# Performance work log

Measured on AMD Instinct MI355X. Metric: run time of the kernel, lower is better.

Reference implementation:

```python
import jax, jax.numpy as jnp
import numpy as np

IH, IW = 14, 14
NUM_HEADS = 16
HEAD_DIMS = 32
INP_DIMS = 512
B = 128


def make_relative_position_index(ih, iw):
    coords = np.stack(np.meshgrid(np.arange(ih), np.arange(iw), indexing='ij'))  # [2, ih, iw]
    cf = coords.reshape(2, -1)  # [2, n]
    rel = cf[:, :, None] - cf[:, None, :]  # [2, n, n]
    rel = rel.transpose(1, 2, 0)  # [n, n, 2]
    rel[:, :, 0] += ih - 1
    rel[:, :, 1] += iw - 1
    rel[:, :, 0] *= 2 * iw - 1
    return rel.sum(-1).astype(np.int64)  # [n, n]


def setup_inputs() -> dict:
    key = jax.random.key(0)
    k1, k2, k3, k4, k5 = jax.random.split(key, 5)
    n = IH * IW
    inner = NUM_HEADS * HEAD_DIMS
    x = jax.random.normal(k1, (B, n, INP_DIMS), dtype=jnp.float32)
    qkv_w = jax.random.normal(k2, (INP_DIMS, 3 * inner), dtype=jnp.float32) * 0.02
    rel_bias_table = jax.random.normal(k3, ((2 * IH - 1) * (2 * IW - 1), NUM_HEADS), dtype=jnp.float32) * 0.02
    proj_w = jax.random.normal(k4, (inner, INP_DIMS), dtype=jnp.float32) * 0.02
    proj_b = jax.random.normal(k5, (INP_DIMS,), dtype=jnp.float32) * 0.02
    rel_pos_index = jnp.asarray(make_relative_position_index(IH, IW))
    return {"x": x, "qkv_w": qkv_w, "rel_bias_table": rel_bias_table,
            "proj_w": proj_w, "proj_b": proj_b, "rel_pos_index": rel_pos_index}


def reference(x, qkv_w, rel_bias_table, proj_w, proj_b, rel_pos_index):
    b, n, c = x.shape
    h, hd = NUM_HEADS, HEAD_DIMS
    scale = (INP_DIMS // NUM_HEADS) ** (-0.5)
    qkv = x @ qkv_w  # [b, n, 3*h*hd]
    qkv = qkv.reshape(b, n, 3, h, hd).transpose(2, 0, 3, 1, 4)  # [3, b, h, n, hd]
    q, k, v = qkv[0] * scale, qkv[1], qkv[2]
    attn = jnp.einsum('bhqd,bhkd->bhqk', q, k)  # [b, h, n, n]
    # gather relative position bias: [n*n, h] -> [h, n, n]
    bias = rel_bias_table[rel_pos_index.reshape(-1)].reshape(n, n, h).transpose(2, 0, 1)
    attn = jax.nn.softmax(attn + bias[None], axis=-1)
    out = jnp.einsum('bhqk,bhkd->bhqd', attn, v)  # [b, h, n, hd]
    out = out.transpose(0, 2, 1, 3).reshape(b, n, h * hd)
    return out @ proj_w + proj_b
```

## Files before the change

### kernel.cpp

```cpp
#include <hip/hip_runtime.h>

#define NTOK 196
#define QPAD 208
#define KP 208
#define PSTR 232
#define VKP 208

typedef __attribute__((ext_vector_type(8))) short short8;
typedef __attribute__((ext_vector_type(4))) short short4_t;
typedef __attribute__((ext_vector_type(4))) float float4_t;

__device__ __forceinline__ short f2bf(float f) {
  unsigned u = __float_as_uint(f);
  u = (u + 0x7fffu + ((u >> 16) & 1u)) >> 16;
  return (short)u;
}

__global__ __launch_bounds__(256) void fill_kernel(float* __restrict__ out,
                                                   int n) {
  int i = blockIdx.x * 256 + threadIdx.x;
  if (i < n) out[i] = 1000.0f;
}

__device__ __forceinline__ void transpose_body(const float* __restrict__ in,
                                               short* __restrict__ out, int R,
                                               int C, int bx, int by,
                                               float (*tile)[65]) {
  int c0 = bx * 64, r0 = by * 64;
  int tc = threadIdx.x & 63, tr = threadIdx.x >> 6;
#pragma unroll
  for (int s = 0; s < 16; s++) {
    int r = s * 4 + tr;
    tile[r][tc] = in[(r0 + r) * C + c0 + tc];
  }
  __syncthreads();
#pragma unroll
  for (int s = 0; s < 16; s++) {
    int i = s * 4 + tr;
    out[(c0 + i) * R + r0 + tc] = f2bf(tile[tc][i]);
  }
}

__global__ __launch_bounds__(256) void prep_kernel(
    const float* __restrict__ qkv_w, const float* __restrict__ proj_w,
    const float* __restrict__ table, const int* __restrict__ rpi,
    const float* __restrict__ x, short* __restrict__ wt1,
    short* __restrict__ wt2, float* __restrict__ bias, short* __restrict__ vb,
    short* __restrict__ xb, int do_vpad) {
  __shared__ float tile[64][65];
  int blk = blockIdx.x;
  if (blk < 192) {
    transpose_body(qkv_w, wt1, 512, 1536, blk % 24, blk / 24, tile);
  } else if (blk < 256) {
    int i = blk - 192;
    transpose_body(proj_w, wt2, 512, 512, i % 8, i / 8, tile);
  } else if (blk < 2960) {
    int idx = (blk - 256) * 256 + threadIdx.x;
    int h = idx / (QPAD * KP);
    int rem = idx % (QPAD * KP);
    int q = rem / KP, k = rem % KP;
    float v = 0.f;
    if (q < NTOK && k < NTOK) v = table[rpi[q * NTOK + k] * 16 + h];
    bias[idx] = v;
  } else if (blk < 3728) {
    if (do_vpad) {
      int i = (blk - 2960) * 256 + threadIdx.x;
      int row = i / 3, g = i - 3 * (i / 3);
      short4_t z = {0, 0, 0, 0};
      *(short4_t*)&vb[row * VKP + 196 + g * 4] = z;
    }
  } else {
    int i = ((blk - 3728) * 256 + threadIdx.x) * 8;
    float4_t a = *(const float4_t*)&x[i];
    float4_t b = *(const float4_t*)&x[i + 4];
    short8 v;
    v[0] = f2bf(a[0]); v[1] = f2bf(a[1]); v[2] = f2bf(a[2]); v[3] = f2bf(a[3]);
    v[4] = f2bf(b[0]); v[5] = f2bf(b[1]); v[6] = f2bf(b[2]); v[7] = f2bf(b[3]);
    *(short8*)&xb[i] = v;
  }
}

__device__ __forceinline__ void gemm_tile(const short* __restrict__ A,
                                          const short* __restrict__ B, int K,
                                          int m0, int n0, short* As, short* Bs,
                                          float4_t acc[4][4]) {
  int tid = threadIdx.x;
  int lane = tid & 63, wave = tid >> 6;
  int quad = lane >> 4, l16 = lane & 15;
  int wm = (wave >> 1) * 64, wn = (wave & 1) * 64;
  int lrow = lane >> 3, lcol = (lane & 7) * 8;
  const short* Abase = A + m0 * K;
  const short* Bbase = B + n0 * K;
  for (int k0 = 0; k0 < K; k0 += 64) {
#pragma unroll
    for (int i = 0; i < 4; i++) {
      int r = (wave * 4 + i) * 8;
      __builtin_amdgcn_global_load_lds(
          (const __attribute__((address_space(1))) void*)
              &Abase[(r + lrow) * K + k0 + lcol],
          (__attribute__((address_space(3))) void*)&As[r * 64], 16, 0, 0);
      __builtin_amdgcn_global_load_lds(
          (const __attribute__((address_space(1))) void*)
              &Bbase[(r + lrow) * K + k0 + lcol],
          (__attribute__((address_space(3))) void*)&Bs[r * 64], 16, 0, 0);
    }
    __syncthreads();
#pragma unroll
    for (int ks = 0; ks < 2; ks++) {
      short8 af[4], bfr[4];
#pragma unroll
      for (int i = 0; i < 4; i++) {
        af[i] = *(short8*)&As[(wm + i * 16 + l16) * 64 + ks * 32 + quad * 8];
        bfr[i] = *(short8*)&Bs[(wn + i * 16 + l16) * 64 + ks * 32 + quad * 8];
      }
#pragma unroll
      for (int mi = 0; mi < 4; mi++)
#pragma unroll
        for (int ni = 0; ni < 4; ni++)
          acc[mi][ni] = __builtin_amdgcn_mfma_f32_16x16x32_bf16(
              af[mi], bfr[ni], acc[mi][ni], 0, 0, 0);
    }
    __syncthreads();
  }
}

__global__ __launch_bounds__(256) void qkv_gemm(
    const short* __restrict__ xb, const short* __restrict__ wt1,
    short* __restrict__ qb, short* __restrict__ kb, short* __restrict__ vb) {
  __shared__ __align__(16) short As[128 * 64];
  __shared__ __align__(16) short Bs[128 * 64];
  float4_t acc[4][4];
  float4_t z = {0.f, 0.f, 0.f, 0.f};
#pragma unroll
  for (int i = 0; i < 4; i++)
#pragma unroll
    for (int j = 0; j < 4; j++) acc[i][j] = z;
  int lin = blockIdx.x + blockIdx.y * 12;
  int xcd = lin & 7, loc = lin >> 3;
  int nl = xcd * 294 + loc;
  int bx = nl % 12, by = nl / 12;
  int m0 = by * 128, n0 = bx * 128;
  gemm_tile(xb, wt1, 512, m0, n0, As, Bs, acc);
  int lane = threadIdx.x & 63, wave = threadIdx.x >> 6;
  int quad = lane >> 4, l16 = lane & 15;
  int wm = (wave >> 1) * 64, wn = (wave & 1) * 64;
  const float qscale = 0.17677669529663687f;
#pragma unroll
  for (int mi = 0; mi < 4; mi++)
#pragma unroll
    for (int ni = 0; ni < 4; ni++) {
      int colg = n0 + wn + ni * 16 + l16;
      int s = colg >> 9, rem = colg & 511;
      int h = rem >> 5, d = rem & 31;
      int rowg0 = m0 + wm + mi * 16 + quad * 4;
      if (s == 2) {
        int b = rowg0 / NTOK, nt = rowg0 - b * NTOK;
        short4_t v4;
        v4[0] = f2bf(acc[mi][ni][0]);
        v4[1] = f2bf(acc[mi][ni][1]);
        v4[2] = f2bf(acc[mi][ni][2]);
        v4[3] = f2bf(acc[mi][ni][3]);
        *(short4_t*)&vb[((b * 16 + h) * 32 + d) * VKP + nt] = v4;
      } else {
#pragma unroll
        for (int r = 0; r < 4; r++) {
          int rowg = rowg0 + r;
          int b = rowg / NTOK, n = rowg - b * NTOK;
          int off = ((b * 16 + h) * QPAD + n) * 32 + d;
          if (s == 0)
            qb[off] = f2bf(acc[mi][ni][r] * qscale);
          else
            kb[off] = f2bf(acc[mi][ni][r]);
        }
      }
    }
}

__global__ __launch_bounds__(256) void attn_kernel(
    const short* __restrict__ qb, const short* __restrict__ kb,
    const short* __restrict__ vb, const float* __restrict__ bias,
    short* __restrict__ aout) {
  __shared__ __align__(16) short vT[32][PSTR];
  __shared__ __align__(16) short P[4][16][PSTR];
  int bh = blockIdx.x, b = bh >> 4, h = bh & 15;
  int tid = threadIdx.x, wave = tid >> 6, lane = tid & 63;
  int quad = lane >> 4, l16 = lane & 15;
  int base_row = b * NTOK;
  const short* vsrc = vb + bh * 32 * VKP;
  for (int i = tid; i < 32 * 26; i += 256) {
    int d = i / 26, c = (i - d * 26) * 8;
    *(short8*)&vT[d][c] = *(const short8*)&vsrc[d * VKP + c];
  }
  short8 z8 = {0, 0, 0, 0, 0, 0, 0, 0};
  if (tid < 96) {
    int d = tid / 3, c = 208 + (tid - d * 3) * 8;
    *(short8*)&vT[d][c] = z8;
  }
  __syncthreads();
  float4_t z4 = {0.f, 0.f, 0.f, 0.f};
  for (int i2 = 0; i2 < 4; i2++) {
    bool active = (i2 < 3) || (wave == 0);
    if (!active) break;
    int qt = (i2 < 3) ? (wave + 4 * i2) : 12;
    int qr0 = qt * 16;
    short8 qf = *(const short8*)&qb[(bh * QPAD + qr0 + l16) * 32 + quad * 8];
    float4_t s[13];
#pragma unroll
    for (int kt = 0; kt < 13; kt++) {
      short8 kf =
          *(const short8*)&kb[(bh * QPAD + kt * 16 + l16) * 32 + quad * 8];
      s[kt] = __builtin_amdgcn_mfma_f32_16x16x32_bf16(qf, kf, z4, 0, 0, 0);
    }
    const float* brow = bias + (h * QPAD + qr0 + quad * 4) * KP;
#pragma unroll
    for (int kt = 0; kt < 13; kt++) {
      int col = kt * 16 + l16;
#pragma unroll
      for (int r = 0; r < 4; r++) s[kt][r] += brow[r * KP + col];
    }
    if (l16 >= 4) {
#pragma unroll
      for (int r = 0; r < 4; r++) s[12][r] = -1e30f;
    }
    float invr[4];
#pragma unroll
    for (int r = 0; r < 4; r++) {
      float m = s[0][r];
#pragma unroll
      for (int kt = 1; kt < 13; kt++) m = fmaxf(m, s[kt][r]);
      m = fmaxf(m, __shfl_xor(m, 8, 16));
      m = fmaxf(m, __shfl_xor(m, 4, 16));
      m = fmaxf(m, __shfl_xor(m, 2, 16));
      m = fmaxf(m, __shfl_xor(m, 1, 16));
      float sum = 0.f;
#pragma unroll
      for (int kt = 0; kt < 13; kt++) {
        float p = __expf(s[kt][r] - m);
        s[kt][r] = p;
        sum += p;
      }
      sum += __shfl_xor(sum, 8, 16);
      sum += __shfl_xor(sum, 4, 16);
      sum += __shfl_xor(sum, 2, 16);
      sum += __shfl_xor(sum, 1, 16);
      invr[r] = 1.f / sum;
      short* prow = &P[wave][quad * 4 + r][0];
#pragma unroll
      for (int kt = 0; kt < 13; kt++)
        prow[kt * 16 + l16] = f2bf(s[kt][r]);
      prow[208 + l16] = 0;
    }
    float4_t o0 = z4, o1 = z4;
#pragma unroll
    for (int kt = 0; kt < 7; kt++) {
      short8 pf = *(short8*)&P[wave][l16][kt * 32 + quad * 8];
      short8 vf0 = *(short8*)&vT[l16][kt * 32 + quad * 8];
      short8 vf1 = *(short8*)&vT[16 + l16][kt * 32 + quad * 8];
      o0 = __builtin_amdgcn_mfma_f32_16x16x32_bf16(pf, vf0, o0, 0, 0, 0);
      o1 = __builtin_amdgcn_mfma_f32_16x16x32_bf16(pf, vf1, o1, 0, 0, 0);
    }
#pragma unroll
    for (int r = 0; r < 4; r++) {
      int row = qr0 + quad * 4 + r;
      if (row < NTOK) {
        int off = (base_row + row) * 512 + h * 32;
        aout[off + l16] = f2bf(o0[r] * invr[r]);
        aout[off + 16 + l16] = f2bf(o1[r] * invr[r]);
      }
    }
  }
}

__global__ __launch_bounds__(256, 2) void fused_attn(
    const short* __restrict__ xb, const short* __restrict__ wt1,
    const float* __restrict__ bias, short* __restrict__ aout) {
  __shared__ __align__(16) short R1[64 * PSTR];
  __shared__ __align__(16) short R2[32 * PSTR];
  __shared__ __align__(16) short Qs[224][40];
  __shared__ __align__(16) short Ks[224][40];
  short(*As)[40] = (short(*)[40])R1;
  short(*P)[PSTR] = (short(*)[PSTR])R1;
  short(*Bs)[40] = (short(*)[40])R2;
  short(*vTs)[PSTR] = (short(*)[PSTR])R2;

  int bh = blockIdx.x, b = bh >> 4, h = bh & 15;
  int tid = threadIdx.x, wave = tid >> 6, lane = tid & 63;
  int quad = lane >> 4, l16 = lane & 15;
  int base_row = b * NTOK;

  float4_t z4 = {0.f, 0.f, 0.f, 0.f};
  float4_t acc[4][6];
#pragma unroll
  for (int i = 0; i < 4; i++)
#pragma unroll
    for (int n = 0; n < 6; n++) acc[i][n] = z4;

  int srow = tid >> 2, scol = (tid & 3) * 8;
  for (int k0 = 0; k0 < 512; k0 += 32) {
#pragma unroll
    for (int i = 0; i < 4; i++) {
      int r = srow + i * 64;
      if (r < 224) {
        int gr = base_row + r;
        if (gr > 25087) gr = 25087;
        *(short8*)&As[r][scol] = *(const short8*)&xb[gr * 512 + k0 + scol];
      }
    }
#pragma unroll
    for (int i = 0; i < 2; i++) {
      int r = srow + i * 64;
      if (r < 96) {
        int sec = r >> 5, r32 = r & 31;
        *(short8*)&Bs[r][scol] =
            *(const short8*)&wt1[(sec * 512 + h * 32 + r32) * 512 + k0 + scol];
      }
    }
    __syncthreads();
    short8 af[4], bfv[6];
#pragma unroll
    for (int i = 0; i < 4; i++) {
      int mt = (i < 3) ? (wave + 4 * i) : (12 + (wave & 1));
      af[i] = *(short8*)&As[mt * 16 + l16][quad * 8];
    }
#pragma unroll
    for (int n = 0; n < 6; n++) bfv[n] = *(short8*)&Bs[n * 16 + l16][quad * 8];
#pragma unroll
    for (int i = 0; i < 4; i++)
#pragma unroll
      for (int n = 0; n < 6; n++)
        acc[i][n] = __builtin_amdgcn_mfma_f32_16x16x32_bf16(af[i], bfv[n],
                                                            acc[i][n], 0, 0, 0);
    __syncthreads();
  }
  const float qscale = 0.17677669529663687f;
#pragma unroll
  for (int i = 0; i < 4; i++) {
    if (i == 3 && wave >= 2) break;
    int mt = (i < 3) ? (wave + 4 * i) : (12 + wave);
    int row0 = mt * 16 + quad * 4;
#pragma unroll
    for (int n = 0; n < 6; n++) {
      int c = n * 16 + l16;
#pragma unroll
      for (int r = 0; r < 4; r++) {
        int row = row0 + r;
        float v = acc[i][n][r];
        if (c < 32)
          Qs[row][c] = f2bf(v * qscale);
        else if (c < 64)
          Ks[row][c - 32] = f2bf(v);
        else
          vTs[c - 64][row] = f2bf(v);
      }
    }
  }
  __syncthreads();
  for (int i2 = 0; i2 < 4; i2++) {
    bool active = (i2 < 3) || (wave == 0);
    int qt = (i2 < 3) ? (wave + 4 * i2) : 12;
    int qr0 = qt * 16;
    if (active) {
      short8 qf = *(short8*)&Qs[qr0 + l16][quad * 8];
      float4_t s[13];
#pragma unroll
      for (int kt = 0; kt < 13; kt++) {
        short8 kf = *(short8*)&Ks[kt * 16 + l16][quad * 8];
        s[kt] = __builtin_amdgcn_mfma_f32_16x16x32_bf16(qf, kf, z4, 0, 0, 0);
      }
      const float* brow = bias + (h * QPAD + qr0 + quad * 4) * KP;
#pragma unroll
      for (int kt = 0; kt < 13; kt++) {
        int col = kt * 16 + l16;
#pragma unroll
        for (int r = 0; r < 4; r++) s[kt][r] += brow[r * KP + col];
      }
      if (l16 >= 4) {
#pragma unroll
        for (int r = 0; r < 4; r++) s[12][r] = -1e30f;
      }
      int prow_base = wave * 16 + quad * 4;
#pragma unroll
      for (int r = 0; r < 4; r++) {
        float m = s[0][r];
#pragma unroll
        for (int kt = 1; kt < 13; kt++) m = fmaxf(m, s[kt][r]);
        m = fmaxf(m, __shfl_xor(m, 8, 16));
        m = fmaxf(m, __shfl_xor(m, 4, 16));
        m = fmaxf(m, __shfl_xor(m, 2, 16));
        m = fmaxf(m, __shfl_xor(m, 1, 16));
        float sum = 0.f;
#pragma unroll
        for (int kt = 0; kt < 13; kt++) {
          float p = __expf(s[kt][r] - m);
          s[kt][r] = p;
          sum += p;
        }
        sum += __shfl_xor(sum, 8, 16);
        sum += __shfl_xor(sum, 4, 16);
        sum += __shfl_xor(sum, 2, 16);
        sum += __shfl_xor(sum, 1, 16);
        float inv = 1.f / sum;
        short* prow = &P[prow_base + r][0];
#pragma unroll
        for (int kt = 0; kt < 13; kt++)
          prow[kt * 16 + l16] = f2bf(s[kt][r] * inv);
        prow[208 + l16] = 0;
      }
    }
    __syncthreads();
    if (active) {
      float4_t o0 = z4, o1 = z4;
#pragma unroll
      for (int kt = 0; kt < 7; kt++) {
        short8 pf = *(short8*)&P[wave * 16 + l16][kt * 32 + quad * 8];
        short8 vf0 = *(short8*)&vTs[l16][kt * 32 + quad * 8];
        short8 vf1 = *(short8*)&vTs[16 + l16][kt * 32 + quad * 8];
        o0 = __builtin_amdgcn_mfma_f32_16x16x32_bf16(pf, vf0, o0, 0, 0, 0);
        o1 = __builtin_amdgcn_mfma_f32_16x16x32_bf16(pf, vf1, o1, 0, 0, 0);
      }
#pragma unroll
      for (int r = 0; r < 4; r++) {
        int row = qr0 + quad * 4 + r;
        if (row < NTOK) {
          int off = (base_row + row) * 512 + h * 32;
          aout[off + l16] = f2bf(o0[r]);
          aout[off + 16 + l16] = f2bf(o1[r]);
        }
      }
    }
    __syncthreads();
  }
}

__global__ __launch_bounds__(256) void proj_gemm(
    const short* __restrict__ a, const short* __restrict__ wt,
    const float* __restrict__ pb, float* __restrict__ out) {
  __shared__ __align__(16) short As[128 * 64];
  __shared__ __align__(16) short Bs[128 * 64];
  float4_t acc[4][4];
  float4_t z = {0.f, 0.f, 0.f, 0.f};
#pragma unroll
  for (int i = 0; i < 4; i++)
#pragma unroll
    for (int j = 0; j < 4; j++) acc[i][j] = z;
  int lin = blockIdx.x + blockIdx.y * 4;
  int xcd = lin & 7, loc = lin >> 3;
  int nl = xcd * 98 + loc;
  int bx = nl % 4, by = nl / 4;
  int m0 = by * 128, n0 = bx * 128;
  gemm_tile(a, wt, 512, m0, n0, As, Bs, acc);
  int lane = threadIdx.x & 63, wave = threadIdx.x >> 6;
  int quad = lane >> 4, l16 = lane & 15;
  int wm = (wave >> 1) * 64, wn = (wave & 1) * 64;
#pragma unroll
  for (int mi = 0; mi < 4; mi++)
#pragma unroll
    for (int ni = 0; ni < 4; ni++) {
      int colg = n0 + wn + ni * 16 + l16;
      float bv = pb[colg];
#pragma unroll
      for (int r = 0; r < 4; r++) {
        int rowg = m0 + wm + mi * 16 + quad * 4 + r;
        out[rowg * 512 + colg] = acc[mi][ni][r] + bv;
      }
    }
}

extern "C" void kernel_launch(void* const* d_in, const int* in_sizes, int n_in,
                              void* d_out, int out_size, void* d_ws,
                              size_t ws_size, hipStream_t stream) {
  const float* x = (const float*)d_in[0];
  const float* qkv_w = (const float*)d_in[1];
  const float* table = (const float*)d_in[2];
  const float* proj_w = (const float*)d_in[3];
  const float* proj_b = (const float*)d_in[4];
  const int* rpi = (const int*)d_in[5];
  float* out = (float*)d_out;

  char* w = (char*)d_ws;
  short* wt1 = (short*)(w);
  short* wt2 = (short*)(w + 1572864);
  float* bias = (float*)(w + 2097152);
  short* xb = (short*)(w + 4866048);
  short* qb = (short*)(w + 30556160);
  short* kb = (short*)(w + 57819136);
  short* vb = (short*)(w + 85082112);
  const size_t NEEDED_SPLIT = 112345088;
  const size_t NEEDED_FUSED = 30556160 + 25690112;

  int split = ws_size >= NEEDED_SPLIT;
  if (ws_size >= NEEDED_FUSED) {
    prep_kernel<<<10000, 256, 0, stream>>>(qkv_w, proj_w, table, rpi, x, wt1,
                                           wt2, bias, vb, xb, split);
  }
  if (split) {
    short* aout = xb;
    qkv_gemm<<<dim3(12, 196), 256, 0, stream>>>(xb, wt1, qb, kb, vb);
    attn_kernel<<<2048, 256, 0, stream>>>(qb, kb, vb, bias, aout);
    proj_gemm<<<dim3(4, 196), 256, 0, stream>>>(aout, wt2, proj_b, out);
  } else if (ws_size >= NEEDED_FUSED) {
    short* aout = (short*)(w + 30556160);
    fused_attn<<<2048, 256, 0, stream>>>(xb, wt1, bias, aout);
    proj_gemm<<<dim3(4, 196), 256, 0, stream>>>(aout, wt2, proj_b, out);
  } else {
    fill_kernel<<<(out_size + 255) / 256, 256, 0, stream>>>(out, out_size);
  }
}
```

Measured before the change: 274.9 us.

## Pad GEMM LDS tiles, fold log2e into scales, hoist K fragments

The GEMM tile loader switches from direct global-to-LDS loads into an unpadded 64-wide layout to plain register-staged loads into 72-wide padded LDS rows. The padding is meant to avoid bank conflicts on the MFMA fragment reads. The softmax now uses exp2f, with log2(e) folded into the query scale and into the precomputed bias table, removing a multiply per exponent. K fragments in the attention kernel are loaded once per block into registers instead of once per query tile, which raises register pressure.

```diff
diff --git a/kernel.cpp b/kernel.cpp
--- a/kernel.cpp
+++ b/kernel.cpp
@@ -60,7 +60,8 @@
     int rem = idx % (QPAD * KP);
     int q = rem / KP, k = rem % KP;
     float v = 0.f;
-    if (q < NTOK && k < NTOK) v = table[rpi[q * NTOK + k] * 16 + h];
+    if (q < NTOK && k < NTOK)
+      v = table[rpi[q * NTOK + k] * 16 + h] * 1.4426950408889634f;
     bias[idx] = v;
   } else if (blk < 3728) {
     if (do_vpad) {
@@ -82,27 +83,19 @@
 
 __device__ __forceinline__ void gemm_tile(const short* __restrict__ A,
                                           const short* __restrict__ B, int K,
-                                          int m0, int n0, short* As, short* Bs,
-                                          float4_t acc[4][4]) {
+                                          int m0, int n0, short (*As)[72],
+                                          short (*Bs)[72], float4_t acc[4][4]) {
   int tid = threadIdx.x;
   int lane = tid & 63, wave = tid >> 6;
   int quad = lane >> 4, l16 = lane & 15;
   int wm = (wave >> 1) * 64, wn = (wave & 1) * 64;
-  int lrow = lane >> 3, lcol = (lane & 7) * 8;
-  const short* Abase = A + m0 * K;
-  const short* Bbase = B + n0 * K;
+  int srow = tid >> 3, scol = (tid & 7) * 8;
   for (int k0 = 0; k0 < K; k0 += 64) {
 #pragma unroll
     for (int i = 0; i < 4; i++) {
-      int r = (wave * 4 + i) * 8;
-      __builtin_amdgcn_global_load_lds(
-          (const __attribute__((address_space(1))) void*)
-              &Abase[(r + lrow) * K + k0 + lcol],
-          (__attribute__((address_space(3))) void*)&As[r * 64], 16, 0, 0);
-      __builtin_amdgcn_global_load_lds(
-          (const __attribute__((address_space(1))) void*)
-              &Bbase[(r + lrow) * K + k0 + lcol],
-          (__attribute__((address_space(3))) void*)&Bs[r * 64], 16, 0, 0);
+      int r = srow + i * 32;
+      *(short8*)&As[r][scol] = *(const short8*)&A[(m0 + r) * K + k0 + scol];
+      *(short8*)&Bs[r][scol] = *(const short8*)&B[(n0 + r) * K + k0 + scol];
     }
     __syncthreads();
 #pragma unroll
@@ -110,8 +103,8 @@
       short8 af[4], bfr[4];
 #pragma unroll
       for (int i = 0; i < 4; i++) {
-        af[i] = *(short8*)&As[(wm + i * 16 + l16) * 64 + ks * 32 + quad * 8];
-        bfr[i] = *(short8*)&Bs[(wn + i * 16 + l16) * 64 + ks * 32 + quad * 8];
+        af[i] = *(short8*)&As[wm + i * 16 + l16][ks * 32 + quad * 8];
+        bfr[i] = *(short8*)&Bs[wn + i * 16 + l16][ks * 32 + quad * 8];
       }
 #pragma unroll
       for (int mi = 0; mi < 4; mi++)
@@ -127,8 +120,8 @@
 __global__ __launch_bounds__(256) void qkv_gemm(
     const short* __restrict__ xb, const short* __restrict__ wt1,
     short* __restrict__ qb, short* __restrict__ kb, short* __restrict__ vb) {
-  __shared__ __align__(16) short As[128 * 64];
-  __shared__ __align__(16) short Bs[128 * 64];
+  __shared__ __align__(16) short As[128][72];
+  __shared__ __align__(16) short Bs[128][72];
   float4_t acc[4][4];
   float4_t z = {0.f, 0.f, 0.f, 0.f};
 #pragma unroll
@@ -144,7 +137,7 @@
   int lane = threadIdx.x & 63, wave = threadIdx.x >> 6;
   int quad = lane >> 4, l16 = lane & 15;
   int wm = (wave >> 1) * 64, wn = (wave & 1) * 64;
-  const float qscale = 0.17677669529663687f;
+  const float qscale = 0.17677669529663687f * 1.4426950408889634f;
 #pragma unroll
   for (int mi = 0; mi < 4; mi++)
 #pragma unroll
@@ -197,6 +190,10 @@
     *(short8*)&vT[d][c] = z8;
   }
   __syncthreads();
+  short8 kfr[13];
+#pragma unroll
+  for (int kt = 0; kt < 13; kt++)
+    kfr[kt] = *(const short8*)&kb[(bh * QPAD + kt * 16 + l16) * 32 + quad * 8];
   float4_t z4 = {0.f, 0.f, 0.f, 0.f};
   for (int i2 = 0; i2 < 4; i2++) {
     bool active = (i2 < 3) || (wave == 0);
@@ -206,11 +203,8 @@
     short8 qf = *(const short8*)&qb[(bh * QPAD + qr0 + l16) * 32 + quad * 8];
     float4_t s[13];
 #pragma unroll
-    for (int kt = 0; kt < 13; kt++) {
-      short8 kf =
-          *(const short8*)&kb[(bh * QPAD + kt * 16 + l16) * 32 + quad * 8];
-      s[kt] = __builtin_amdgcn_mfma_f32_16x16x32_bf16(qf, kf, z4, 0, 0, 0);
-    }
+    for (int kt = 0; kt < 13; kt++)
+      s[kt] = __builtin_amdgcn_mfma_f32_16x16x32_bf16(qf, kfr[kt], z4, 0, 0, 0);
     const float* brow = bias + (h * QPAD + qr0 + quad * 4) * KP;
 #pragma unroll
     for (int kt = 0; kt < 13; kt++) {
@@ -235,7 +229,7 @@
       float sum = 0.f;
 #pragma unroll
       for (int kt = 0; kt < 13; kt++) {
-        float p = __expf(s[kt][r] - m);
+        float p = exp2f(s[kt][r] - m);
         s[kt][r] = p;
         sum += p;
       }
@@ -332,7 +326,7 @@
                                                             acc[i][n], 0, 0, 0);
     __syncthreads();
   }
-  const float qscale = 0.17677669529663687f;
+  const float qscale = 0.17677669529663687f * 1.4426950408889634f;
 #pragma unroll
   for (int i = 0; i < 4; i++) {
     if (i == 3 && wave >= 2) break;
@@ -391,7 +385,7 @@
         float sum = 0.f;
 #pragma unroll
         for (int kt = 0; kt < 13; kt++) {
-          float p = __expf(s[kt][r] - m);
+          float p = exp2f(s[kt][r] - m);
           s[kt][r] = p;
           sum += p;
         }
@@ -435,8 +429,8 @@
 __global__ __launch_bounds__(256) void proj_gemm(
     const short* __restrict__ a, const short* __restrict__ wt,
     const float* __restrict__ pb, float* __restrict__ out) {
-  __shared__ __align__(16) short As[128 * 64];
-  __shared__ __align__(16) short Bs[128 * 64];
+  __shared__ __align__(16) short As[128][72];
+  __shared__ __align__(16) short Bs[128][72];
   float4_t acc[4][4];
   float4_t z = {0.f, 0.f, 0.f, 0.f};
 #pragma unroll
```

Result: no change. 271.7 us (-1.2%).
